# Performance work log

Hardware: AMD Instinct MI355X
Metric: run time of the kernel (lower is better)

The kernel has to match this reference:

```python
import jax, jax.numpy as jnp
import numpy as np

M = 15
WIN = 5  # tension detector window_size
SIGMA = 0.1
_ZETA = np.array([14.134725, 21.02204, 25.010858, 30.424876, 32.935062,
                  37.586178, 40.91872, 43.327073, 48.005151, 49.773832,
                  52.970321, 56.446248, 59.347044, 60.831779, 65.112544], dtype=np.float32)
GAMMAS = jnp.asarray(_ZETA)                       # [M]
PHI = jnp.asarray(np.exp(-SIGMA * np.abs(_ZETA)).astype(np.float32))  # [M]

B, S, I, H = 256, 512, 256, 512


def setup_inputs() -> dict:
    key = jax.random.key(0)
    ks = jax.random.split(key, 12)
    s_i = 1.0 / np.sqrt(I)
    s_h = 1.0 / np.sqrt(H)
    return {
        "x": jax.random.normal(ks[0], (B, S, I), dtype=jnp.float32),
        # LSTMCell params (PyTorch layout: gates i,f,g,o)
        "W_ih": jax.random.normal(ks[1], (4 * H, I), dtype=jnp.float32) * s_i,
        "W_hh": jax.random.normal(ks[2], (4 * H, H), dtype=jnp.float32) * s_h,
        "b_ih": jax.random.normal(ks[3], (4 * H,), dtype=jnp.float32) * s_h,
        "b_hh": jax.random.normal(ks[4], (4 * H,), dtype=jnp.float32) * s_h,
        # spectrum analyzer input_proj: Linear(I -> 2M)
        "W_proj": jax.random.normal(ks[5], (2 * M, I), dtype=jnp.float32) * s_i,
        "b_proj": jax.random.normal(ks[6], (2 * M,), dtype=jnp.float32) * s_i,
        # tension detector change_detector: Linear(2H->H), ReLU, Linear(H->1), Sigmoid
        "W_t1": jax.random.normal(ks[7], (H, 2 * H), dtype=jnp.float32) * (1.0 / np.sqrt(2 * H)),
        "b_t1": jax.random.normal(ks[8], (H,), dtype=jnp.float32) * s_h,
        "W_t2": jax.random.normal(ks[9], (1, H), dtype=jnp.float32) * s_h,
        "b_t2": jax.random.normal(ks[10], (1,), dtype=jnp.float32) * s_h,
        # zeta memory gate_combiner: Linear(2 -> 1)
        "W_g": jax.random.normal(ks[11], (1, 2), dtype=jnp.float32) * 0.5,
        "b_g": jnp.zeros((1,), dtype=jnp.float32),
    }


def _forward(x, W_ih, W_hh, b_ih, b_hh, W_proj, b_proj, W_t1, b_t1, W_t2, b_t2, W_g, b_g):
    batch = x.shape[0]
    seq_len = x.shape[1]
    hid = W_hh.shape[1]

    h0 = jnp.zeros((batch, hid), dtype=x.dtype)
    c0 = jnp.zeros((batch, hid), dtype=x.dtype)
    hist0 = jnp.zeros((batch, WIN, hid), dtype=x.dtype)

    def step(carry, inp):
        h, c, hist = carry
        x_t, t = inp                      # x_t: [B, I], t: scalar int
        tf = t.astype(x.dtype)

        # LSTMCell (produces h_new, c_new)
        gates = x_t @ W_ih.T + b_ih + h @ W_hh.T + b_hh   # [B, 4H]
        gi, gf, gg, go = jnp.split(gates, 4, axis=1)
        c_new = jax.nn.sigmoid(gf) * c + jax.nn.sigmoid(gi) * jnp.tanh(gg)
        h_new = jax.nn.sigmoid(go) * jnp.tanh(c_new)

        # ZetaSpectrumAnalyzer on x_t
        proj = x_t @ W_proj.T + b_proj                     # [B, 2M]
        cos_coeffs, sin_coeffs = proj[:, :M], proj[:, M:]
        zc = jnp.cos(GAMMAS * tf)                          # [M]
        zs = jnp.sin(GAMMAS * tf)
        cos_corr = jnp.sum(cos_coeffs * zc * PHI, axis=1)
        sin_corr = jnp.sum(sin_coeffs * zs * PHI, axis=1)
        resonance = jax.nn.sigmoid(jnp.sqrt(cos_corr**2 + sin_corr**2 + 1e-8) - 0.5)[:, None]  # [B,1]

        # TensionMarkerDetector on OLD h (history stores detached old h)
        hist = hist.at[:, t % WIN].set(jax.lax.stop_gradient(h))
        h_mean = hist.mean(axis=1)                         # [B, H]
        comp = jnp.concatenate([h, h_mean], axis=1)        # [B, 2H]
        tension = jax.nn.sigmoid(jax.nn.relu(comp @ W_t1.T + b_t1) @ W_t2.T + b_t2)  # [B,1]
        tension = jnp.where(t < 2, jnp.zeros_like(tension), tension)

        # ZetaMemoryGated on OLD h
        zeta_weight = jnp.sum(PHI * jnp.cos(GAMMAS * tf)) / M  # scalar
        m_raw = zeta_weight * h                                # [B, H]
        gate_in = jnp.concatenate([resonance, tension], axis=1)  # [B, 2]
        gate = jax.nn.sigmoid(gate_in @ W_g.T + b_g)             # [B, 1]
        h_out = h_new + gate * m_raw

        return (h_out, c_new, hist), h_out

    xs = (jnp.swapaxes(x, 0, 1), jnp.arange(seq_len, dtype=jnp.int32))
    (h_n, c_n, _), ys = jax.lax.scan(step, (h0, c0, hist0), xs)
    output = jnp.swapaxes(ys, 0, 1)        # [B, S, H]
    return output, h_n[None], c_n[None]


def reference(x, W_ih, W_hh, b_ih, b_hh, W_proj, b_proj, W_t1, b_t1, W_t2, b_t2, W_g, b_g):
    return _forward(x, W_ih, W_hh, b_ih, b_hh, W_proj, b_proj, W_t1, b_t1, W_t2, b_t2, W_g, b_g)
```

## Files before the change

kernel.cpp:

```cpp
#include <hip/hip_runtime.h>

typedef _Float16 f16;
typedef _Float16 f16x8 __attribute__((ext_vector_type(8)));
typedef float f32x4 __attribute__((ext_vector_type(4)));
typedef float f32x2 __attribute__((ext_vector_type(2)));
typedef unsigned long long u64;

#define DEVFN static __device__ __forceinline__

#define NBLK 256

#define OFF_WCAT 0ULL
#define OFF_WT1A (OFF_WCAT + 2048ULL*768*2)
#define OFF_WT1B (OFF_WT1A + 512ULL*512*2)
#define OFF_HB0  (OFF_WT1B + 512ULL*512*2)
#define OFF_HB1  (OFF_HB0  + 256ULL*512*2)
#define OFF_BSUM (OFF_HB1  + 256ULL*512*2)
#define OFF_U    (OFF_BSUM + 2048ULL*4)
#define OFF_V    (OFF_U    + 512ULL*256*4)
#define OFF_CU   (OFF_V    + 512ULL*256*4)
#define OFF_CV   (OFF_CU   + 512ULL*4)
#define OFF_ZETA (OFF_CV   + 512ULL*4)
#define OFF_RES  (OFF_ZETA + 512ULL*4)
#define OFF_TENSP (OFF_RES + 512ULL*256*4)
#define OFF_SLOT (OFF_TENSP + 16384ULL*4)

__constant__ float CGAM[15] = {14.134725f, 21.02204f, 25.010858f, 30.424876f, 32.935062f,
  37.586178f, 40.91872f, 43.327073f, 48.005151f, 49.773832f, 52.970321f,
  56.446248f, 59.347044f, 60.831779f, 65.112544f};

DEVFN float sigf(float v) { return 1.f / (1.f + __expf(-v)); }
DEVFN float tanh_(float v) {
  v = fminf(fmaxf(v, -15.f), 15.f);
  float e = __expf(2.f * v);
  return (e - 1.f) / (e + 1.f);
}

DEVFN float ald_f32(const float* p) {
  unsigned v = __hip_atomic_load((const unsigned*)p, __ATOMIC_RELAXED, __HIP_MEMORY_SCOPE_AGENT);
  union { unsigned u; float f; } c; c.u = v; return c.f;
}
DEVFN void ast_f32(float* p, float v) {
  union { float f; unsigned u; } c; c.f = v;
  __hip_atomic_store((unsigned*)p, c.u, __ATOMIC_RELAXED, __HIP_MEMORY_SCOPE_AGENT);
}
DEVFN u64 ald_u64(const void* p) {
  return __hip_atomic_load((const u64*)p, __ATOMIC_RELAXED, __HIP_MEMORY_SCOPE_AGENT);
}
DEVFN void ast_u32(void* p, unsigned v) {
  __hip_atomic_store((unsigned*)p, v, __ATOMIC_RELAXED, __HIP_MEMORY_SCOPE_AGENT);
}

DEVFN void post(unsigned* slot, unsigned v) {
  asm volatile("s_waitcnt vmcnt(0)" ::: "memory");
  __syncthreads();
  if (threadIdx.x == 0)
    __hip_atomic_store(slot, v, __ATOMIC_RELAXED, __HIP_MEMORY_SCOPE_AGENT);
}
DEVFN void wait_line(const unsigned* line, unsigned target) {
  const unsigned* pp = line + (threadIdx.x & 31);
  long sp = 0;
  for (;;) {
    unsigned v = __hip_atomic_load(pp, __ATOMIC_RELAXED, __HIP_MEMORY_SCOPE_AGENT);
    if (__all(v >= target)) break;
    __builtin_amdgcn_s_sleep(1);
    if (++sp > (1L << 21)) break;
  }
}

__global__ void k_init(const float* __restrict__ x, const float* __restrict__ Wih,
                       const float* __restrict__ Whh, const float* __restrict__ bih,
                       const float* __restrict__ bhh, const float* __restrict__ Wt1f,
                       char* __restrict__ ws) {
  f16* Wcat = (f16*)(ws + OFF_WCAT);
  f16* WhmA = (f16*)(ws + OFF_WT1A);
  f16* WmB  = (f16*)(ws + OFF_WT1B);
  f16* hb0  = (f16*)(ws + OFF_HB0);
  float* bsum = (float*)(ws + OFF_BSUM);
  float* tensP = (float*)(ws + OFF_TENSP);
  unsigned* slots = (unsigned*)(ws + OFF_SLOT);
  int gtid = blockIdx.x * blockDim.x + threadIdx.x;
  int nth = gridDim.x * blockDim.x;
  for (int i = gtid; i < 2048 * 768; i += nth) {
    int n = i / 768, k = i - n * 768;
    float w = (k < 256) ? Wih[n * 256 + k] : Whh[n * 512 + (k - 256)];
    Wcat[i] = (f16)w;
  }
  for (int i = gtid; i < 512 * 512; i += nth) {
    int n = i >> 9, k = i & 511;
    float wh = Wt1f[n * 1024 + k];
    float wm = Wt1f[n * 1024 + 512 + k] * 0.2f;
    WhmA[i] = (f16)(wh + wm);
    WmB[i]  = (f16)wm;
  }
  for (int i = gtid; i < 2048; i += nth) bsum[i] = bih[i] + bhh[i];
  for (int i = gtid; i < 256 * 512; i += nth) hb0[i] = (f16)0.f;
  for (int i = gtid; i < 16384; i += nth) tensP[i] = 0.f;
  for (int i = gtid; i < 8 * 64; i += nth) slots[i] = 0u;
}

__global__ void k_tables(const float* __restrict__ Wproj, const float* __restrict__ bproj,
                         char* __restrict__ ws) {
  float* u    = (float*)(ws + OFF_U);
  float* v    = (float*)(ws + OFF_V);
  float* cu   = (float*)(ws + OFF_CU);
  float* cv   = (float*)(ws + OFF_CV);
  float* zeta = (float*)(ws + OFF_ZETA);
  int t = blockIdx.x;
  int k = threadIdx.x;
  float tf = (float)t;
  float cg[15], sg[15], ph[15];
  #pragma unroll
  for (int m = 0; m < 15; ++m) {
    float ang = CGAM[m] * tf;
    cg[m] = cosf(ang);
    sg[m] = sinf(ang);
    ph[m] = (float)exp(-0.1 * (double)CGAM[m]);
  }
  float uu = 0.f, vv = 0.f;
  #pragma unroll
  for (int m = 0; m < 15; ++m) {
    uu += Wproj[m * 256 + k] * cg[m] * ph[m];
    vv += Wproj[(15 + m) * 256 + k] * sg[m] * ph[m];
  }
  u[t * 256 + k] = uu;
  v[t * 256 + k] = vv;
  if (k == 0) {
    float a = 0.f, b2 = 0.f, z = 0.f;
    #pragma unroll
    for (int m = 0; m < 15; ++m) {
      a  += bproj[m] * cg[m] * ph[m];
      b2 += bproj[15 + m] * sg[m] * ph[m];
      z  += ph[m] * cg[m];
    }
    cu[t] = a; cv[t] = b2; zeta[t] = z / 15.f;
  }
}

__global__ void k_res(const float* __restrict__ x, char* __restrict__ ws) {
  const float* u  = (const float*)(ws + OFF_U);
  const float* v  = (const float*)(ws + OFF_V);
  const float* cu = (const float*)(ws + OFF_CU);
  const float* cv = (const float*)(ws + OFF_CV);
  float* resb     = (float*)(ws + OFF_RES);
  int wid = blockIdx.x * 4 + (threadIdx.x >> 6);
  int l = threadIdx.x & 63;
  int b = wid >> 9, t = wid & 511;
  const f32x4 xx = *(const f32x4*)(x + ((size_t)(b * 512 + t)) * 256 + l * 4);
  const f32x4 uu = *(const f32x4*)(u + t * 256 + l * 4);
  const f32x4 vv = *(const f32x4*)(v + t * 256 + l * 4);
  float cc = xx[0]*uu[0] + xx[1]*uu[1] + xx[2]*uu[2] + xx[3]*uu[3];
  float ss = xx[0]*vv[0] + xx[1]*vv[1] + xx[2]*vv[2] + xx[3]*vv[3];
  #pragma unroll
  for (int m = 1; m < 64; m <<= 1) { cc += __shfl_xor(cc, m); ss += __shfl_xor(ss, m); }
  if (l == 0) {
    cc += cu[t]; ss += cv[t];
    float r = sqrtf(cc * cc + ss * ss + 1e-8f) - 0.5f;
    resb[t * 256 + b] = sigf(r);
  }
}

#define MFMA16(qv, wv, av) av = __builtin_amdgcn_mfma_f32_16x16x32_f16(qv, wv, av, 0, 0, 0)

__global__ void __launch_bounds__(256, 1)
k_lstm(const float* __restrict__ x, const float* __restrict__ bt1,
       const float* __restrict__ wt2, const float* __restrict__ bt2,
       const float* __restrict__ wg, const float* __restrict__ bg,
       float* __restrict__ out, char* __restrict__ ws) {
  extern __shared__ char lds[];
  char*  sH   = lds;
  char*  sXt0 = lds + 32768;
  char*  sXt1 = lds + 49152;
  float* sT   = (float*)(lds + 65536);
  float* sX   = (float*)(lds + 74752);
  float* sGZ  = (float*)(lds + 84992);

  const f16* __restrict__ Wcat = (const f16*)(ws + OFF_WCAT);
  const f16* __restrict__ WhmA = (const f16*)(ws + OFF_WT1A);
  const f16* __restrict__ WmB  = (const f16*)(ws + OFF_WT1B);
  f16* hb[2] = { (f16*)(ws + OFF_HB0), (f16*)(ws + OFF_HB1) };
  const float* bsum = (const float*)(ws + OFF_BSUM);
  const float* zeta = (const float*)(ws + OFF_ZETA);
  const float* resb = (const float*)(ws + OFF_RES);
  float* tensP = (float*)(ws + OFF_TENSP);
  unsigned* slots = (unsigned*)(ws + OFF_SLOT);

  const int tid = threadIdx.x;
  const int w = tid >> 6, l = tid & 63;
  const int r0 = l & 15, kq = l >> 4;
  const int bid = blockIdx.x;
  const int p = bid >> 5, q = bid & 31;
  const int c0 = q * 16, m0 = p * 32;

  unsigned* slotH = slots + p * 64;
  unsigned* myH = slotH + q;

  f16x8 wbh[16], wbx[8];
  {
    const f16* Wr = Wcat + (size_t)(w * 512 + c0 + r0) * 768 + kq * 8;
    #pragma unroll
    for (int ks = 0; ks < 16; ++ks) wbh[ks] = *(const f16x8*)(Wr + 256 + ks * 32);
    #pragma unroll
    for (int ks = 0; ks < 8; ++ks)  wbx[ks] = *(const f16x8*)(Wr + ks * 32);
  }
  f16x8 wbhm[4], wbm[4];
  {
    const f16* Wa = WhmA + (size_t)(q * 16 + r0) * 512 + w * 128 + kq * 8;
    const f16* Wb = WmB  + (size_t)(q * 16 + r0) * 512 + w * 128 + kq * 8;
    #pragma unroll
    for (int ks = 0; ks < 4; ++ks) {
      wbhm[ks] = *(const f16x8*)(Wa + ks * 32);
      wbm[ks]  = *(const f16x8*)(Wb + ks * 32);
    }
  }
  const float b1a = bt1[q * 16 + r0], w2a = wt2[q * 16 + r0];

  const int b_loc = tid >> 3, c_loc = (tid & 7) * 2;
  const int pb = m0 + b_loc;
  float bsv[4][2];
  #pragma unroll
  for (int g = 0; g < 4; ++g) {
    bsv[g][0] = bsum[g * 512 + c0 + c_loc];
    bsv[g][1] = bsum[g * 512 + c0 + c_loc + 1];
  }
  const float wg0 = wg[0], wg1 = wg[1], bt2v = bt2[0], bgv = bg[0];
  float cst[2] = {0.f, 0.f};
  float hst[2] = {0.f, 0.f};
  float hnp[2] = {0.f, 0.f};

  f32x4 gho0 = {0,0,0,0}, gho1 = {0,0,0,0};
  f32x4 t1o0 = {0,0,0,0}, t1o1 = {0,0,0,0};
  f32x4 R[4][2];
  #pragma unroll
  for (int s = 0; s < 4; ++s) { R[s][0] = (f32x4){0,0,0,0}; R[s][1] = (f32x4){0,0,0,0}; }

  f32x4 ppx0 = {0,0,0,0}, ppx1 = {0,0,0,0};
  {
    #pragma unroll
    for (int i = 0; i < 4; ++i) {
      const int U = i * 256 + tid;
      const int row = U >> 5, c = U & 31;
      const float* xp = x + ((size_t)(m0 + row) * 512 + 0) * 256 + c * 8;
      f32x4 xa = *(const f32x4*)xp;
      f32x4 xb_ = *(const f32x4*)(xp + 4);
      f16x8 xf;
      #pragma unroll
      for (int r = 0; r < 4; ++r) { xf[r] = (f16)xa[r]; xf[4 + r] = (f16)xb_[r]; }
      *(f16x8*)(sXt0 + row * 512 + ((c ^ (row & 7)) << 4)) = xf;
    }
    __syncthreads();
    #pragma unroll
    for (int ks = 0; ks < 8; ++ks) {
      const int cc = (((ks * 4 + kq) ^ (r0 & 7)) << 4);
      f16x8 a0 = *(const f16x8*)(sXt0 + r0 * 512 + cc);
      f16x8 a1 = *(const f16x8*)(sXt0 + (r0 + 16) * 512 + cc);
      MFMA16(a0, wbx[ks], ppx0); MFMA16(a1, wbx[ks], ppx1);
    }
    #pragma unroll
    for (int i = 0; i < 4; ++i) {
      const int U = i * 256 + tid;
      const int row = U >> 5, c = U & 31;
      const float* xp = x + ((size_t)(m0 + row) * 512 + 1) * 256 + c * 8;
      f32x4 xa = *(const f32x4*)xp;
      f32x4 xb_ = *(const f32x4*)(xp + 4);
      f16x8 xf;
      #pragma unroll
      for (int r = 0; r < 4; ++r) { xf[r] = (f16)xa[r]; xf[4 + r] = (f16)xb_[r]; }
      *(f16x8*)(sXt1 + row * 512 + ((c ^ (row & 7)) << 4)) = xf;
    }
    __syncthreads();
  }

  for (int t = 0; t < 512; ++t) {
    const int par = t & 1, parm = (t - 1) & 1;

    wait_line(slotH, (unsigned)t);

    u64 lo[8], hi[8];
    if (t > 0) {
      const f16* hsrc = hb[parm];
      #pragma unroll
      for (int i = 0; i < 8; ++i) {
        const int B = i * 256 + tid;
        const int row = B >> 6, c = B & 63;
        const u64* pp = (const u64*)(hsrc + (size_t)(m0 + row) * 512 + c * 8);
        lo[i] = ald_u64(pp); hi[i] = ald_u64(pp + 1);
      }
    }

    {
      float tn = 0.f;
      if (t >= 3) {
        const float* tpb = tensP + ((size_t)parm * 8 + p) * 1024;
        const int s8 = tid & 7;
        float acc = 0.f;
        #pragma unroll
        for (int j2 = 0; j2 < 4; ++j2)
          acc += ald_f32(tpb + (s8 * 4 + j2) * 32 + b_loc);
        acc += __shfl_xor(acc, 1); acc += __shfl_xor(acc, 2); acc += __shfl_xor(acc, 4);
        tn = sigf(acc + bt2v);
      }
      float g = 0.f;
      if (t >= 1) {
        float rs = resb[(t - 1) * 256 + pb];
        g = sigf(wg0 * rs + wg1 * tn + bgv) * zeta[t - 1];
      }
      if ((tid & 7) == 0) sGZ[b_loc] = g;
    }

    if (t > 0) {
      #pragma unroll
      for (int i = 0; i < 8; ++i) {
        const int B = i * 256 + tid;
        const int row = B >> 6, c = B & 63;
        union { u64 qq[2]; uint4 v4; } uq; uq.qq[0] = lo[i]; uq.qq[1] = hi[i];
        *(uint4*)(sH + row * 1024 + ((c ^ (row & 7)) << 4)) = uq.v4;
      }
    }
    __syncthreads();

    f32x4 ghn0 = {0,0,0,0}, ghn1 = {0,0,0,0};
    f32x4 t1n0 = {0,0,0,0}, t1n1 = {0,0,0,0};
    f32x4 cnw0 = {0,0,0,0}, cnw1 = {0,0,0,0};
    if (t > 0) {
      #pragma unroll
      for (int ks = 0; ks < 16; ++ks) {
        const int cc = (((ks * 4 + kq) ^ (r0 & 7)) << 4);
        f16x8 q0 = *(const f16x8*)(sH + r0 * 1024 + cc);
        f16x8 q1 = *(const f16x8*)(sH + (r0 + 16) * 1024 + cc);
        MFMA16(q0, wbh[ks], ghn0); MFMA16(q1, wbh[ks], ghn1);
      }
      #pragma unroll
      for (int ks = 0; ks < 4; ++ks) {
        const int cc = ((((w * 4 + ks) * 4 + kq) ^ (r0 & 7)) << 4);
        f16x8 q0 = *(const f16x8*)(sH + r0 * 1024 + cc);
        f16x8 q1 = *(const f16x8*)(sH + (r0 + 16) * 1024 + cc);
        MFMA16(q0, wbhm[ks], t1n0); MFMA16(q1, wbhm[ks], t1n1);
        MFMA16(q0, wbm[ks],  cnw0); MFMA16(q1, wbm[ks],  cnw1);
      }
    }

    {
      float gz0[4], gz1[4];
      #pragma unroll
      for (int r = 0; r < 4; ++r) { gz0[r] = sGZ[kq * 4 + r]; gz1[r] = sGZ[16 + kq * 4 + r]; }
      f32x4 co0, co1, tp0, tp1;
      #pragma unroll
      for (int r = 0; r < 4; ++r) {
        gho0[r] = ghn0[r] + gz0[r] * gho0[r];
        gho1[r] = ghn1[r] + gz1[r] * gho1[r];
        t1o0[r] = t1n0[r] + gz0[r] * t1o0[r];
        t1o1[r] = t1n1[r] + gz1[r] * t1o1[r];
        co0[r] = cnw0[r] + gz0[r] * R[0][0][r];
        co1[r] = cnw1[r] + gz1[r] * R[0][1][r];
        tp0[r] = t1o0[r] + R[0][0][r] + R[1][0][r] + R[2][0][r] + R[3][0][r];
        tp1[r] = t1o1[r] + R[0][1][r] + R[1][1][r] + R[2][1][r] + R[3][1][r];
      }
      #pragma unroll
      for (int s = 3; s > 0; --s) { R[s][0] = R[s - 1][0]; R[s][1] = R[s - 1][1]; }
      R[0][0] = co0; R[0][1] = co1;
      const int rb = kq * 4;
      float* tpx = sT + w * 576 + l * 9;
      #pragma unroll
      for (int r = 0; r < 4; ++r) {
        sX[(w * 32 + rb + r) * 20 + r0]      = ppx0[r] + gho0[r];
        sX[(w * 32 + 16 + rb + r) * 20 + r0] = ppx1[r] + gho1[r];
        tpx[r] = tp0[r]; tpx[4 + r] = tp1[r];
      }
    }
    __syncthreads();

    {
      const int rf0 = w * 2;
      #pragma unroll
      for (int rr = 0; rr < 2; ++rr) {
        const int rf = rf0 + rr;
        float v = sT[l * 9 + rf] + sT[576 + l * 9 + rf]
                + sT[1152 + l * 9 + rf] + sT[1728 + l * 9 + rf] + b1a;
        float s = fmaxf(v, 0.f) * w2a;
        s += __shfl_xor(s, 1); s += __shfl_xor(s, 2);
        s += __shfl_xor(s, 4); s += __shfl_xor(s, 8);
        if (r0 == 0) {
          int row = (rf < 4) ? (kq * 4 + rf) : (16 + kq * 4 + (rf - 4));
          ast_f32(tensP + (((size_t)par * 8 + p) * 32 + q) * 32 + row, s);
        }
      }
    }

    float hn_[2];
    #pragma unroll
    for (int e = 0; e < 2; ++e) {
      float gi = sX[(      b_loc) * 20 + c_loc + e] + bsv[0][e];
      float gf = sX[( 32 + b_loc) * 20 + c_loc + e] + bsv[1][e];
      float gg = sX[( 64 + b_loc) * 20 + c_loc + e] + bsv[2][e];
      float go = sX[( 96 + b_loc) * 20 + c_loc + e] + bsv[3][e];
      float c_new = sigf(gf) * cst[e] + sigf(gi) * tanh_(gg);
      cst[e] = c_new;
      hn_[e] = sigf(go) * tanh_(c_new);
    }
    float gzb = sGZ[b_loc];
    float hop[2] = { hnp[0] + gzb * hst[0], hnp[1] + gzb * hst[1] };
    {
      union { f16 h2[2]; unsigned u; } ph_;
      ph_.h2[0] = (f16)hn_[0]; ph_.h2[1] = (f16)hn_[1];
      ast_u32(hb[par] + (size_t)pb * 512 + c0 + c_loc, ph_.u);
    }
    post(myH, (unsigned)(t + 1));

    if (t >= 1) {
      f32x2 ov = {hop[0], hop[1]};
      *(f32x2*)(out + ((size_t)pb * 512 + (t - 1)) * 512 + c0 + c_loc) = ov;
    }
    hst[0] = hop[0]; hst[1] = hop[1];
    hnp[0] = hn_[0]; hnp[1] = hn_[1];
    if (t < 511) {
      char* sXcur = (((t + 1) & 1) ? sXt1 : sXt0);
      ppx0 = (f32x4){0,0,0,0}; ppx1 = (f32x4){0,0,0,0};
      #pragma unroll
      for (int ks = 0; ks < 8; ++ks) {
        const int cc = (((ks * 4 + kq) ^ (r0 & 7)) << 4);
        f16x8 a0 = *(const f16x8*)(sXcur + r0 * 512 + cc);
        f16x8 a1 = *(const f16x8*)(sXcur + (r0 + 16) * 512 + cc);
        MFMA16(a0, wbx[ks], ppx0); MFMA16(a1, wbx[ks], ppx1);
      }
      if (t < 510) {
        char* sXnxt = ((t & 1) ? sXt1 : sXt0);
        #pragma unroll
        for (int i = 0; i < 4; ++i) {
          const int U = i * 256 + tid;
          const int row = U >> 5, c = U & 31;
          const float* xp = x + ((size_t)(m0 + row) * 512 + (t + 2)) * 256 + c * 8;
          f32x4 xa = *(const f32x4*)xp;
          f32x4 xb_ = *(const f32x4*)(xp + 4);
          f16x8 xf;
          #pragma unroll
          for (int r = 0; r < 4; ++r) { xf[r] = (f16)xa[r]; xf[4 + r] = (f16)xb_[r]; }
          *(f16x8*)(sXnxt + row * 512 + ((c ^ (row & 7)) << 4)) = xf;
        }
      }
    }
  }

  wait_line(slotH, 512u);
  {
    const float* tpb = tensP + ((size_t)(511 & 1) * 8 + p) * 1024;
    const int s8 = tid & 7;
    float acc = 0.f;
    #pragma unroll
    for (int j2 = 0; j2 < 4; ++j2)
      acc += ald_f32(tpb + (s8 * 4 + j2) * 32 + b_loc);
    acc += __shfl_xor(acc, 1); acc += __shfl_xor(acc, 2); acc += __shfl_xor(acc, 4);
    float tn = sigf(acc + bt2v);
    float rs = resb[511 * 256 + pb];
    float gzb = sigf(wg0 * rs + wg1 * tn + bgv) * zeta[511];
    float hop[2] = { hnp[0] + gzb * hst[0], hnp[1] + gzb * hst[1] };
    f32x2 ov = {hop[0], hop[1]};
    *(f32x2*)(out + ((size_t)pb * 512 + 511) * 512 + c0 + c_loc) = ov;
    *(f32x2*)(out + 67108864 + (size_t)pb * 512 + c0 + c_loc) = ov;
    f32x2 cv2 = {cst[0], cst[1]};
    *(f32x2*)(out + 67108864 + 131072 + (size_t)pb * 512 + c0 + c_loc) = cv2;
  }
}

extern "C" void kernel_launch(void* const* d_in, const int* in_sizes, int n_in,
                              void* d_out, int out_size, void* d_ws, size_t ws_size,
                              hipStream_t stream) {
  (void)in_sizes; (void)n_in; (void)out_size; (void)ws_size;
  const float* x     = (const float*)d_in[0];
  const float* Wih   = (const float*)d_in[1];
  const float* Whh   = (const float*)d_in[2];
  const float* bih   = (const float*)d_in[3];
  const float* bhh   = (const float*)d_in[4];
  const float* Wproj = (const float*)d_in[5];
  const float* bproj = (const float*)d_in[6];
  const float* Wt1   = (const float*)d_in[7];
  const float* bt1   = (const float*)d_in[8];
  const float* Wt2   = (const float*)d_in[9];
  const float* bt2   = (const float*)d_in[10];
  const float* Wg    = (const float*)d_in[11];
  const float* bg    = (const float*)d_in[12];
  float* out = (float*)d_out;
  char* ws = (char*)d_ws;
  hipFuncSetAttribute((const void*)k_lstm, hipFuncAttributeMaxDynamicSharedMemorySize, 131072);
  k_init<<<dim3(1024), dim3(256), 0, stream>>>(x, Wih, Whh, bih, bhh, Wt1, ws);
  k_tables<<<dim3(512), dim3(256), 0, stream>>>(Wproj, bproj, ws);
  k_res<<<dim3(32768), dim3(256), 0, stream>>>(x, ws);
  k_lstm<<<dim3(NBLK), dim3(256), 85120, stream>>>(x, bt1, Wt2, bt2, Wg, bg, out, ws);
}
```

Baseline: 3.240 ms.

## Replace block barrier and flag with per-wave flags and speculative polling

Each wave now posts its own completion flag, so the barrier before publishing the hidden-state slice is gone. Waiting blocks poll 128 per-wave flags per group and speculatively read them before the x-projection MFMA work, so the poll is skipped when all producers are already done. sGZ is double-buffered by step parity to avoid the race the removed barrier used to prevent. The cost is more flag traffic per poll and a wider flag array, plus slightly more shared memory.

```diff
diff --git a/kernel.cpp b/kernel.cpp
--- a/kernel.cpp
+++ b/kernel.cpp
@@ -50,19 +50,22 @@
 DEVFN void ast_u32(void* p, unsigned v) {
   __hip_atomic_store((unsigned*)p, v, __ATOMIC_RELAXED, __HIP_MEMORY_SCOPE_AGENT);
 }
-
-DEVFN void post(unsigned* slot, unsigned v) {
+DEVFN unsigned ald_u32(const void* p) {
+  return __hip_atomic_load((const unsigned*)p, __ATOMIC_RELAXED, __HIP_MEMORY_SCOPE_AGENT);
+}
+
+DEVFN void post_wave(unsigned* subslot, unsigned v, int lane) {
   asm volatile("s_waitcnt vmcnt(0)" ::: "memory");
-  __syncthreads();
-  if (threadIdx.x == 0)
-    __hip_atomic_store(slot, v, __ATOMIC_RELAXED, __HIP_MEMORY_SCOPE_AGENT);
-}
-DEVFN void wait_line(const unsigned* line, unsigned target) {
-  const unsigned* pp = line + (threadIdx.x & 31);
+  if (lane == 0)
+    __hip_atomic_store(subslot, v, __ATOMIC_RELAXED, __HIP_MEMORY_SCOPE_AGENT);
+}
+DEVFN void poll_line128(const unsigned* base, unsigned target, int lane) {
+  const unsigned* p0 = base + lane;
+  const unsigned* p1 = base + 64 + lane;
   long sp = 0;
   for (;;) {
-    unsigned v = __hip_atomic_load(pp, __ATOMIC_RELAXED, __HIP_MEMORY_SCOPE_AGENT);
-    if (__all(v >= target)) break;
+    unsigned v0 = ald_u32(p0), v1 = ald_u32(p1);
+    if (__all((v0 >= target) & (v1 >= target))) break;
     __builtin_amdgcn_s_sleep(1);
     if (++sp > (1L << 21)) break;
   }
@@ -96,7 +99,7 @@
   for (int i = gtid; i < 2048; i += nth) bsum[i] = bih[i] + bhh[i];
   for (int i = gtid; i < 256 * 512; i += nth) hb0[i] = (f16)0.f;
   for (int i = gtid; i < 16384; i += nth) tensP[i] = 0.f;
-  for (int i = gtid; i < 8 * 64; i += nth) slots[i] = 0u;
+  for (int i = gtid; i < 8 * 128; i += nth) slots[i] = 0u;
 }
 
 __global__ void k_tables(const float* __restrict__ Wproj, const float* __restrict__ bproj,
@@ -192,8 +195,8 @@
   const int p = bid >> 5, q = bid & 31;
   const int c0 = q * 16, m0 = p * 32;
 
-  unsigned* slotH = slots + p * 64;
-  unsigned* myH = slotH + q;
+  unsigned* slotB = slots + p * 128;
+  unsigned* mySlot = slotB + q * 4 + w;
 
   f16x8 wbh[16], wbx[8];
   {
@@ -271,10 +274,13 @@
     __syncthreads();
   }
 
+  unsigned spec0 = 0u, spec1 = 0u;
+
   for (int t = 0; t < 512; ++t) {
     const int par = t & 1, parm = (t - 1) & 1;
 
-    wait_line(slotH, (unsigned)t);
+    if (!__all((spec0 >= (unsigned)t) & (spec1 >= (unsigned)t)))
+      poll_line128(slotB, (unsigned)t, l);
 
     u64 lo[8], hi[8];
     if (t > 0) {
@@ -305,7 +311,7 @@
         float rs = resb[(t - 1) * 256 + pb];
         g = sigf(wg0 * rs + wg1 * tn + bgv) * zeta[t - 1];
       }
-      if ((tid & 7) == 0) sGZ[b_loc] = g;
+      if ((tid & 7) == 0) sGZ[par * 32 + b_loc] = g;
     }
 
     if (t > 0) {
@@ -343,7 +349,10 @@
     {
       float gz0[4], gz1[4];
       #pragma unroll
-      for (int r = 0; r < 4; ++r) { gz0[r] = sGZ[kq * 4 + r]; gz1[r] = sGZ[16 + kq * 4 + r]; }
+      for (int r = 0; r < 4; ++r) {
+        gz0[r] = sGZ[par * 32 + kq * 4 + r];
+        gz1[r] = sGZ[par * 32 + 16 + kq * 4 + r];
+      }
       f32x4 co0, co1, tp0, tp1;
       #pragma unroll
       for (int r = 0; r < 4; ++r) {
@@ -398,14 +407,14 @@
       cst[e] = c_new;
       hn_[e] = sigf(go) * tanh_(c_new);
     }
-    float gzb = sGZ[b_loc];
+    float gzb = sGZ[par * 32 + b_loc];
     float hop[2] = { hnp[0] + gzb * hst[0], hnp[1] + gzb * hst[1] };
     {
       union { f16 h2[2]; unsigned u; } ph_;
       ph_.h2[0] = (f16)hn_[0]; ph_.h2[1] = (f16)hn_[1];
       ast_u32(hb[par] + (size_t)pb * 512 + c0 + c_loc, ph_.u);
     }
-    post(myH, (unsigned)(t + 1));
+    post_wave(mySlot, (unsigned)(t + 1), l);
 
     if (t >= 1) {
       f32x2 ov = {hop[0], hop[1]};
@@ -413,6 +422,8 @@
     }
     hst[0] = hop[0]; hst[1] = hop[1];
     hnp[0] = hn_[0]; hnp[1] = hn_[1];
+    spec0 = ald_u32(slotB + l);
+    spec1 = ald_u32(slotB + 64 + l);
     if (t < 511) {
       char* sXcur = (((t + 1) & 1) ? sXt1 : sXt0);
       ppx0 = (f32x4){0,0,0,0}; ppx1 = (f32x4){0,0,0,0};
@@ -441,7 +452,8 @@
     }
   }
 
-  wait_line(slotH, 512u);
+  if (!__all((spec0 >= 512u) & (spec1 >= 512u)))
+    poll_line128(slotB, 512u, l);
   {
     const float* tpb = tensP + ((size_t)(511 & 1) * 8 + p) * 1024;
     const int s8 = tid & 7;
@@ -485,5 +497,5 @@
   k_init<<<dim3(1024), dim3(256), 0, stream>>>(x, Wih, Whh, bih, bhh, Wt1, ws);
   k_tables<<<dim3(512), dim3(256), 0, stream>>>(Wproj, bproj, ws);
   k_res<<<dim3(32768), dim3(256), 0, stream>>>(x, ws);
-  k_lstm<<<dim3(NBLK), dim3(256), 85120, stream>>>(x, bt1, Wt2, bt2, Wg, bg, out, ws);
-}
+  k_lstm<<<dim3(NBLK), dim3(256), 85248, stream>>>(x, bt1, Wt2, bt2, Wg, bg, out, ws);
+}
```

Result: slower. 4.132 ms (+27.5%).
